# Kernel optimization log

Measured on AMD Instinct MI355X. Metric: run time of the kernel, lower is better.

The kernel has to match this reference:

```python
import math
import jax, jax.numpy as jnp
import numpy as np

RM = 100.0      # r_max
RN = 1000       # r_dsc
LMAX = 2
MATCH_FRAC = 0.1
PARA1 = 1.0
RD = RM / RN    # radial step
NE = 4096       # batch of trial energies


def setup_inputs() -> dict:
    key = jax.random.key(0)
    # small negative energies (bound-state regime) to keep the exponential
    # Numerov growth over 900 steps within fp32 range
    init_energy = -(jax.random.uniform(key, (NE,), dtype=jnp.float32) * 0.01 + 0.005)
    return {"init_energy": init_energy}


def _disc_solve(sol0, factor, limit):
    # sol0: (5, n_e, L) initial 5-point window; factor: (rn, n_e, L)
    # Numerov-style 4-step recurrence, vectorized coefficients + lax.scan
    c = 3.0 / 40.0 * RD ** 2
    idx = jnp.arange(1, limit - 5)
    f0 = factor[idx]
    f1 = factor[idx + 1]
    f2 = factor[idx + 2]
    f3 = factor[idx + 3]
    f4 = factor[idx + 4]
    denom = 1.0 - c * f4
    a = -1.0 + c * f0 / denom
    b = 2.0 + (13.0 / 15.0) * RD ** 2 * f1 / denom
    cc = -2.0 + (7.0 / 60.0) * RD ** 2 * f2 / denom
    d = 2.0 + (13.0 / 15.0) * RD ** 2 * f3 / denom

    def step(prev, coef):
        ca, cb, ccc, cd = coef
        new4 = ca * prev[1] + cb * prev[2] + ccc * prev[3] + cd * prev[4]
        new = jnp.concatenate([prev[1:], new4[None]], axis=0)  # shift window
        return new, new

    _, rest = jax.lax.scan(step, sol0, (a, b, cc, d))
    return jnp.concatenate([sol0[None], rest], axis=0)  # (limit-5, 5, n_e, L)


def _derivative(func, at):
    return (25.0 * func[at - 1] - 48.0 * func[at - 2] + 36.0 * func[at - 3]
            - 16.0 * func[at - 4] + 3.0 * func[at - 5]) / (12.0 * RD)


def _integrate(func):
    # faithful to original: integrand squares `func` again (func is u**2 here)
    M = func.shape[0] // 4 - 1
    g0 = func[0:4 * M:4]
    g1 = func[1:4 * M:4]
    g2 = func[2:4 * M:4]
    g3 = func[3:4 * M:4]
    g4 = func[4::4][:M]
    integrand = (7.0 * (g0 ** 2 + g4 ** 2) + 32.0 * (g1 ** 2 + g3 ** 2)
                 + 12.0 * g2) * (2.0 * RD / 45.0)
    return integrand.sum(axis=0)


def _forward(init_energy):
    L = LMAX + 1
    dt = init_energy.dtype
    n_e = init_energy.shape[0]
    r = jnp.linspace(RM / RN, RM, RN, dtype=dt).reshape(RN, 1, 1)
    l = jnp.arange(L, dtype=dt).reshape(1, 1, L)

    energy = jnp.broadcast_to(init_energy[:, None], (n_e, L))  # (n_e, L)
    e_val = energy[None]                                       # (1, n_e, L)
    # coulomb potential -1/r; factor: (rn, n_e, L)
    factor = l * (l + 1) / r ** 2 + PARA1 * (-e_val - 1.0 / r)

    # left (r->0) initial window: u ~ r^(l+1) + r^(l+2)/(2(l+1)) * (-para_1)
    r0 = jnp.linspace(RD, 5 * RD, 5, dtype=dt).reshape(5, 1, 1)
    u_zero_init = jnp.broadcast_to(
        r0 ** (l + 1) - r0 ** (l + 2) / (2.0 * (l + 1)) * PARA1, (5, n_e, L))

    # right (r->r_max) initial window: r * truncated spherical-bessel series
    r_inf = jnp.linspace(RM - 4 * RD, RM, 5, dtype=dt).reshape(5, 1, 1)
    fact = jnp.array([math.prod([2 * li + 1 for li in range(lm + 1)])
                      for lm in range(L)], dtype=dt)  # [1, 3, 15]
    x = r_inf * jnp.sqrt(jnp.abs(e_val))              # (5, n_e, L)
    base = x ** l / fact
    t1 = x ** 2 / 2.0 / (2 * l + 3)
    t2 = (x ** 2 / 2.0) ** 2 / (2.0 * (2 * l + 3) * (2 * l + 5))
    u_infty_init = jnp.broadcast_to(r_inf * (base * (1.0 + t1 + t2)), (5, n_e, L))

    match = int(RN * MATCH_FRAC)  # 100
    uz = _disc_solve(u_zero_init, factor, match)                     # (95, 5, n_e, L)
    ui = _disc_solve(u_infty_init, factor[::-1], RN - match)[::-1]   # (895, 5, n_e, L)
    u_zero = jnp.concatenate([uz[0], uz[:, 4]], axis=0)    # (100, n_e, L)
    u_infty = jnp.concatenate([ui[0], ui[:, 4]], axis=0)   # (900, n_e, L)

    lfunc_in = _derivative(u_zero, match) / u_zero[-1]
    # faithful: the trailing flip acts on the energy axis of the (n_e, L) result
    lfunc_out = _derivative(u_infty[::-1], RN - match)[::-1] / u_infty[0]
    integ_in = _integrate(u_zero ** 2)
    integ_out = _integrate(u_infty ** 2)
    delta = -(lfunc_out - lfunc_in) / (integ_in / u_zero[-1] ** 2
                                       + integ_out / u_infty[0] ** 2)
    return (energy + delta, u_zero, u_infty)


def reference(init_energy):
    return _forward(init_energy)
```

## Files before the change

kernel.cpp:

```cpp
#include <hip/hip_runtime.h>


namespace {
constexpr int kNE    = 4096;
constexpr int kNCH   = kNE * 3;
constexpr int kMatch = 100;
constexpr float kC   = 3.0f / 40.0f * 0.01f;
constexpr float kK1  = 13.0f / 15.0f * 0.01f;
constexpr float kK2  = 7.0f / 60.0f * 0.01f;
constexpr int kSeg        = 32;
constexpr int kCPB        = 16;
constexpr int kZeroBlocks = kNCH / 512;
constexpr int kInfBlocks  = kNCH / kCPB;
}

__device__ __forceinline__ float rcp_f(float x) { return __builtin_amdgcn_rcpf(x); }
__device__ __forceinline__ void nt_store(float v, float* p) { __builtin_nontemporal_store(v, p); }

__global__ __launch_bounds__(512) void solve_kernel(const float* __restrict__ energy,
                                                    float* __restrict__ out,
                                                    float* __restrict__ ws)
{
    __shared__ float sP[kSeg][kCPB][16];
    __shared__ float sSt[kSeg][kCPB][4];
    float* sR4 = &sP[0][0][0];
    float* sR2 = sR4 + kSeg * kCPB;

    const int bid = (int)blockIdx.x;
    const int tid = (int)threadIdx.x;
    float* uzero = out + kNCH;
    float* uinf  = out + kNCH + (size_t)kMatch * kNCH;

    if (bid < kZeroBlocks) {
        const int t  = bid * 512 + tid;
        const int l  = t % 3;
        const int ei = t / 3;
        const float e = energy[ei], negE = -e;
        const float ll1 = (float)(l * (l + 1));
        const float rdiv = (l == 0) ? 0.5f : ((l == 1) ? 0.25f : (1.0f/6.0f));
        float p0,p1,p2,p3,p4;
        {
            float pw[5];
            #pragma unroll
            for (int k = 0; k < 5; ++k) {
                float r = 0.1f * (float)(k + 1);
                float rl1 = (l == 0) ? r : ((l == 1) ? r*r : r*r*r);
                pw[k] = rl1 - (rl1 * r) * rdiv;
                nt_store(pw[k], uzero + (size_t)k * kNCH + t);
            }
            nt_store(pw[4], uzero + (size_t)5 * kNCH + t);
            p0=pw[0]; p1=pw[1]; p2=pw[2]; p3=pw[3]; p4=pw[4];
        }
        float acc4, acc2;
        {
            float q0=p0*p0, q1=p1*p1, q2=p2*p2, q3=p3*p3, q4=p4*p4;
            acc4 = 7.0f*q0*q0 + 32.0f*q1*q1 + 32.0f*q3*q3 + 14.0f*q4*q4 + 32.0f*q4*q4;
            acc2 = q2;
        }
        float f0, f1, f2, f3;
        {
            float i1 = rcp_f(0.2f), i2 = rcp_f(0.3f), i3 = rcp_f(0.4f), i4 = rcp_f(0.5f);
            f0 = fmaf(i1, fmaf(ll1, i1, -1.0f), negE);
            f1 = fmaf(i2, fmaf(ll1, i2, -1.0f), negE);
            f2 = fmaf(i3, fmaf(ll1, i3, -1.0f), negE);
            f3 = fmaf(i4, fmaf(ll1, i4, -1.0f), negE);
        }
        float* ptr = uzero + (size_t)6 * kNCH + t;
        #pragma unroll 4
        for (int j = 5; j <= 98; ++j) {
            float ri = rcp_f(fmaf((float)j, 0.1f, 0.1f));
            float f4 = fmaf(ri, fmaf(ll1, ri, -1.0f), negE);
            float iv = rcp_f(fmaf(-kC, f4, 1.0f));
            float a  = fmaf(kC  * f0, iv, -1.0f);
            float b  = fmaf(kK1 * f1, iv,  2.0f);
            float cc = fmaf(kK2 * f2, iv, -2.0f);
            float d  = fmaf(kK1 * f3, iv,  2.0f);
            float nw = fmaf(d, p4, fmaf(cc, p3, fmaf(b, p2, a * p1)));
            nt_store(nw, ptr); ptr += kNCH;
            float v2 = nw*nw, v4 = v2*v2;
            if (j <= 94) {
                int m = (j + 1) & 3;
                if (m == 2)      acc2 += v2;
                else if (m == 0) acc4 += 14.0f * v4;
                else             acc4 += 32.0f * v4;
            } else if (j == 95) {
                acc4 += 7.0f * v4;
            }
            f0 = f1; f1 = f2; f2 = f3; f3 = f4;
            p0 = p1; p1 = p2; p2 = p3; p3 = p4; p4 = nw;
        }
        float integ = fmaf(12.0f, acc2, acc4) * (2.0f * 0.1f / 45.0f);
        float deriv = fmaf(25.0f, p4, fmaf(-48.0f, p3, fmaf(36.0f, p2,
                      fmaf(-16.0f, p1, 3.0f * p0)))) * (1.0f / 1.2f);
        ws[2 * kNCH + t] = deriv / p4;
        ws[3 * kNCH + t] = integ / (p4 * p4);
        return;
    }

    const int b = bid - kZeroBlocks;
    const int g = tid & 15;
    const int s = tid >> 4;
    const int t = b * kCPB + g;
    const int l  = t % 3;
    const int ei = t / 3;
    const float e = energy[ei], negE = -e;
    const float ll1 = (float)(l * (l + 1));
    const int jstart = 5 + 28 * s;
    int j = jstart;

    float F0, F1, F2, F3;
    {
        float i0 = rcp_f(fmaf((float)(jstart - 4), -0.1f, 100.0f));
        float i1 = rcp_f(fmaf((float)(jstart - 3), -0.1f, 100.0f));
        float i2 = rcp_f(fmaf((float)(jstart - 2), -0.1f, 100.0f));
        float i3 = rcp_f(fmaf((float)(jstart - 1), -0.1f, 100.0f));
        F0 = fmaf(i0, fmaf(ll1, i0, -1.0f), negE);
        F1 = fmaf(i1, fmaf(ll1, i1, -1.0f), negE);
        F2 = fmaf(i2, fmaf(ll1, i2, -1.0f), negE);
        F3 = fmaf(i3, fmaf(ll1, i3, -1.0f), negE);
    }
    const float ff0 = F0, ff1 = F1, ff2 = F2, ff3 = F3;

    float ca, cb, cc_, cd;
#define COEF(FA,FB,FC,FD) \
    { float ri = rcp_f(fmaf((float)j, -0.1f, 100.0f)); \
      float f4 = fmaf(ri, fmaf(ll1, ri, -1.0f), negE); \
      float iv = rcp_f(fmaf(-kC, f4, 1.0f)); \
      ca  = fmaf(kC  * FA, iv, -1.0f); \
      cb  = fmaf(kK1 * FB, iv,  2.0f); \
      cc_ = fmaf(kK2 * FC, iv, -2.0f); \
      cd  = fmaf(kK1 * FD, iv,  2.0f); \
      FA = f4; }

#define MSTEP(FA,FB,FC,FD,RA,RB,RC,RD) \
    { COEF(FA,FB,FC,FD) \
      RA[0] = fmaf(cd,RD[0], fmaf(cc_,RC[0], fmaf(cb,RB[0], ca*RA[0]))); \
      RA[1] = fmaf(cd,RD[1], fmaf(cc_,RC[1], fmaf(cb,RB[1], ca*RA[1]))); \
      RA[2] = fmaf(cd,RD[2], fmaf(cc_,RC[2], fmaf(cb,RB[2], ca*RA[2]))); \
      RA[3] = fmaf(cd,RD[3], fmaf(cc_,RC[3], fmaf(cb,RB[3], ca*RA[3]))); \
      ++j; }

    if (s < kSeg - 1) {
        float ra[4] = {1,0,0,0}, rb[4] = {0,1,0,0}, rc[4] = {0,0,1,0}, rd[4] = {0,0,0,1};
        for (int it = 0; it < 7; ++it) {
            MSTEP(F0,F1,F2,F3, ra,rb,rc,rd)
            MSTEP(F1,F2,F3,F0, rb,rc,rd,ra)
            MSTEP(F2,F3,F0,F1, rc,rd,ra,rb)
            MSTEP(F3,F0,F1,F2, rd,ra,rb,rc)
        }
        float* dst = &sP[s][g][0];
        #pragma unroll
        for (int c = 0; c < 4; ++c) {
            dst[c] = ra[c]; dst[4+c] = rb[c]; dst[8+c] = rc[c]; dst[12+c] = rd[c];
        }
    }
    __syncthreads();

    if (s == 0) {
        const float se  = sqrtf(fabsf(e));
        const float rfc = (l == 0) ? 1.0f : ((l == 1) ? (1.0f/3.0f) : (1.0f/15.0f));
        const float rt1 = (l == 0) ? (1.0f/3.0f) : ((l == 1) ? (1.0f/5.0f) : (1.0f/7.0f));
        const float rt2 = (l == 0) ? (1.0f/30.0f) : ((l == 1) ? (1.0f/70.0f) : (1.0f/126.0f));
        float pw[5];
        #pragma unroll
        for (int k = 0; k < 5; ++k) {
            float rinf = 99.6f + 0.1f * (float)k;
            float x  = rinf * se;
            float xl = (l == 0) ? 1.0f : ((l == 1) ? x : x * x);
            float h  = x * x * 0.5f;
            pw[k] = rinf * (xl * rfc * (1.0f + h * rt1 + (h * h) * rt2));
        }
        nt_store(pw[4], uinf + (size_t)899 * kNCH + t);
        float st0 = pw[1], st1 = pw[2], st2 = pw[3], st3 = pw[4];
        for (int ss = 0; ss < kSeg; ++ss) {
            sSt[ss][g][0] = st0; sSt[ss][g][1] = st1;
            sSt[ss][g][2] = st2; sSt[ss][g][3] = st3;
            if (ss < kSeg - 1) {
                const float* P = &sP[ss][g][0];
                float n0 = fmaf(P[ 3],st3, fmaf(P[ 2],st2, fmaf(P[ 1],st1, P[ 0]*st0)));
                float n1 = fmaf(P[ 7],st3, fmaf(P[ 6],st2, fmaf(P[ 5],st1, P[ 4]*st0)));
                float n2 = fmaf(P[11],st3, fmaf(P[10],st2, fmaf(P[ 9],st1, P[ 8]*st0)));
                float n3 = fmaf(P[15],st3, fmaf(P[14],st2, fmaf(P[13],st1, P[12]*st0)));
                st0 = n0; st1 = n1; st2 = n2; st3 = n3;
            }
        }
    }
    __syncthreads();

    j = jstart;
    F0 = ff0; F1 = ff1; F2 = ff2; F3 = ff3;
    float p0 = sSt[s][g][0], p1 = sSt[s][g][1], p2 = sSt[s][g][2], p3 = sSt[s][g][3];
    float acc4 = 0.0f, acc2 = 0.0f;
    float* ptr = uinf + (size_t)(903 - jstart) * kNCH + t;
#define RSTEP(FA,FB,FC,FD,PA,PB,PC,PD) \
    { COEF(FA,FB,FC,FD) \
      float nw = fmaf(cd,PD, fmaf(cc_,PC, fmaf(cb,PB, ca*PA))); \
      PA = nw; nt_store(nw, ptr); ptr -= kNCH; \
      float v2 = nw*nw, v4 = v2*v2; \
      if (j >= 8) { int m = j & 3; \
        if (m == 1) acc2 += v2; \
        else acc4 += ((m == 3) ? 14.0f : 32.0f) * v4; } \
      else if (j == 7) acc4 += 7.0f * v4; \
      ++j; }

    float h0 = 0.0f;
    if (s < kSeg - 1) {
        for (int it = 0; it < 7; ++it) {
            RSTEP(F0,F1,F2,F3, p0,p1,p2,p3)
            RSTEP(F1,F2,F3,F0, p1,p2,p3,p0)
            RSTEP(F2,F3,F0,F1, p2,p3,p0,p1)
            RSTEP(F3,F0,F1,F2, p3,p0,p1,p2)
        }
    } else {
        for (int it = 0; it < 6; ++it) {
            RSTEP(F0,F1,F2,F3, p0,p1,p2,p3)
            RSTEP(F1,F2,F3,F0, p1,p2,p3,p0)
            RSTEP(F2,F3,F0,F1, p2,p3,p0,p1)
            RSTEP(F3,F0,F1,F2, p3,p0,p1,p2)
        }
        RSTEP(F0,F1,F2,F3, p0,p1,p2,p3)
        h0 = p1;
        RSTEP(F1,F2,F3,F0, p1,p2,p3,p0)
    }
    sR4[s * kCPB + g] = acc4;
    sR2[s * kCPB + g] = acc2;
    __syncthreads();

    if (s == kSeg - 1) {
        float a4 = 0.0f, a2 = 0.0f;
        #pragma unroll
        for (int ss = 0; ss < kSeg; ++ss) {
            a4 += sR4[ss * kCPB + g]; a2 += sR2[ss * kCPB + g];
        }
        float h1 = p2, h2 = p3, h3 = p0, h4 = p1;
        nt_store(h0, uinf + (size_t)0 * kNCH + t);
        nt_store(h1, uinf + (size_t)1 * kNCH + t);
        nt_store(h2, uinf + (size_t)2 * kNCH + t);
        nt_store(h3, uinf + (size_t)3 * kNCH + t);
        nt_store(h4, uinf + (size_t)4 * kNCH + t);
        float q0 = h0*h0, q1 = h1*h1, q2 = h2*h2, q3 = h3*h3, q4 = h4*h4;
        a4 += 7.0f*q0*q0 + 32.0f*q1*q1 + 32.0f*q3*q3 + 14.0f*q4*q4;
        a2 += q2;
        float integ = fmaf(12.0f, a2, a4) * (2.0f * 0.1f / 45.0f);
        float deriv = fmaf(25.0f, h0, fmaf(-48.0f, h1, fmaf(36.0f, h2,
                      fmaf(-16.0f, h3, 3.0f * h4)))) * (1.0f / 1.2f);
        ws[t]        = deriv / h0;
        ws[kNCH + t] = integ / (h0 * h0);
    }
#undef RSTEP
#undef MSTEP
#undef COEF
}

__global__ __launch_bounds__(256) void final_kernel(const float* __restrict__ energy,
                                                    const float* __restrict__ ws,
                                                    float* __restrict__ out)
{
    int t = (int)blockIdx.x * 256 + (int)threadIdx.x;
    if (t >= kNCH) return;
    int l = t % 3, ei = t / 3;
    float lf_out = ws[(kNE - 1 - ei) * 3 + l];
    float lf_in  = ws[2 * kNCH + t];
    float den    = ws[kNCH + t] + ws[3 * kNCH + t];
    out[t] = energy[ei] - (lf_out - lf_in) / den;
}

extern "C" void kernel_launch(void* const* d_in, const int* in_sizes, int n_in,
                              void* d_out, int out_size, void* d_ws, size_t ws_size,
                              hipStream_t stream) {
    (void)in_sizes; (void)n_in; (void)out_size; (void)ws_size;
    const float* energy = (const float*)d_in[0];
    float* out = (float*)d_out;
    float* ws  = (float*)d_ws;
    solve_kernel<<<kZeroBlocks + kInfBlocks, 512, 0, stream>>>(energy, out, ws);
    final_kernel<<<kNCH / 256, 256, 0, stream>>>(energy, ws, out);
}
```

Measured before the change: 92.40 us.

## Precompute radial terms in LDS, replace reciprocal with series, transpose sP, drop nontemporal stores

Builds a shared-memory table of the r-dependent potential terms per block, so the inner loops read them instead of computing two hardware reciprocals per step. The 1/(1-c*f) denominator becomes a second-order series, which relies on c*f being tiny at large r. The segment propagator matrices are stored transposed to avoid LDS bank conflicts in the serial combine, and nontemporal stores become ordinary stores. This adds a block-wide table build and sync, and slightly changes numerics.

```diff
diff --git a/kernel.cpp b/kernel.cpp
--- a/kernel.cpp
+++ b/kernel.cpp
@@ -15,15 +15,19 @@
 }
 
 __device__ __forceinline__ float rcp_f(float x) { return __builtin_amdgcn_rcpf(x); }
-__device__ __forceinline__ void nt_store(float v, float* p) { __builtin_nontemporal_store(v, p); }
+__device__ __forceinline__ float rcp_nr(float x) {
+    float r = __builtin_amdgcn_rcpf(x);
+    return fmaf(fmaf(-x, r, 1.0f), r, r);
+}
 
 __global__ __launch_bounds__(512) void solve_kernel(const float* __restrict__ energy,
                                                     float* __restrict__ out,
                                                     float* __restrict__ ws)
 {
-    __shared__ float sP[kSeg][kCPB][16];
+    __shared__ float gt[899 * 3];
+    __shared__ float sPT[16][kSeg - 1][kCPB];
     __shared__ float sSt[kSeg][kCPB][4];
-    float* sR4 = &sP[0][0][0];
+    float* sR4 = &sPT[0][0][0];
     float* sR2 = sR4 + kSeg * kCPB;
 
     const int bid = (int)blockIdx.x;
@@ -46,9 +50,9 @@
                 float r = 0.1f * (float)(k + 1);
                 float rl1 = (l == 0) ? r : ((l == 1) ? r*r : r*r*r);
                 pw[k] = rl1 - (rl1 * r) * rdiv;
-                nt_store(pw[k], uzero + (size_t)k * kNCH + t);
+                uzero[(size_t)k * kNCH + t] = pw[k];
             }
-            nt_store(pw[4], uzero + (size_t)5 * kNCH + t);
+            uzero[(size_t)5 * kNCH + t] = pw[4];
             p0=pw[0]; p1=pw[1]; p2=pw[2]; p3=pw[3]; p4=pw[4];
         }
         float acc4, acc2;
@@ -76,7 +80,7 @@
             float cc = fmaf(kK2 * f2, iv, -2.0f);
             float d  = fmaf(kK1 * f3, iv,  2.0f);
             float nw = fmaf(d, p4, fmaf(cc, p3, fmaf(b, p2, a * p1)));
-            nt_store(nw, ptr); ptr += kNCH;
+            *ptr = nw; ptr += kNCH;
             float v2 = nw*nw, v4 = v2*v2;
             if (j <= 94) {
                 int m = (j + 1) & 3;
@@ -97,6 +101,14 @@
         return;
     }
 
+    for (int j = tid; j < 899; j += 512) {
+        float ri = rcp_nr(fmaf((float)j, -0.1f, 100.0f));
+        gt[j * 3 + 0] = -ri;
+        gt[j * 3 + 1] = ri * fmaf(2.0f, ri, -1.0f);
+        gt[j * 3 + 2] = ri * fmaf(6.0f, ri, -1.0f);
+    }
+    __syncthreads();
+
     const int b = bid - kZeroBlocks;
     const int g = tid & 15;
     const int s = tid >> 4;
@@ -104,28 +116,21 @@
     const int l  = t % 3;
     const int ei = t / 3;
     const float e = energy[ei], negE = -e;
-    const float ll1 = (float)(l * (l + 1));
     const int jstart = 5 + 28 * s;
-    int j = jstart;
-
-    float F0, F1, F2, F3;
-    {
-        float i0 = rcp_f(fmaf((float)(jstart - 4), -0.1f, 100.0f));
-        float i1 = rcp_f(fmaf((float)(jstart - 3), -0.1f, 100.0f));
-        float i2 = rcp_f(fmaf((float)(jstart - 2), -0.1f, 100.0f));
-        float i3 = rcp_f(fmaf((float)(jstart - 1), -0.1f, 100.0f));
-        F0 = fmaf(i0, fmaf(ll1, i0, -1.0f), negE);
-        F1 = fmaf(i1, fmaf(ll1, i1, -1.0f), negE);
-        F2 = fmaf(i2, fmaf(ll1, i2, -1.0f), negE);
-        F3 = fmaf(i3, fmaf(ll1, i3, -1.0f), negE);
-    }
-    const float ff0 = F0, ff1 = F1, ff2 = F2, ff3 = F3;
+
+    const float ff0 = gt[(jstart - 4) * 3 + l] + negE;
+    const float ff1 = gt[(jstart - 3) * 3 + l] + negE;
+    const float ff2 = gt[(jstart - 2) * 3 + l] + negE;
+    const float ff3 = gt[(jstart - 1) * 3 + l] + negE;
+    float F0 = ff0, F1 = ff1, F2 = ff2, F3 = ff3;
+    const float* gp0 = &gt[jstart * 3 + l];
+    const float* gp = gp0;
 
     float ca, cb, cc_, cd;
 #define COEF(FA,FB,FC,FD) \
-    { float ri = rcp_f(fmaf((float)j, -0.1f, 100.0f)); \
-      float f4 = fmaf(ri, fmaf(ll1, ri, -1.0f), negE); \
-      float iv = rcp_f(fmaf(-kC, f4, 1.0f)); \
+    { float f4 = *gp + negE; gp += 3; \
+      float x  = kC * f4; \
+      float iv = fmaf(x, x, x) + 1.0f; \
       ca  = fmaf(kC  * FA, iv, -1.0f); \
       cb  = fmaf(kK1 * FB, iv,  2.0f); \
       cc_ = fmaf(kK2 * FC, iv, -2.0f); \
@@ -137,8 +142,7 @@
       RA[0] = fmaf(cd,RD[0], fmaf(cc_,RC[0], fmaf(cb,RB[0], ca*RA[0]))); \
       RA[1] = fmaf(cd,RD[1], fmaf(cc_,RC[1], fmaf(cb,RB[1], ca*RA[1]))); \
       RA[2] = fmaf(cd,RD[2], fmaf(cc_,RC[2], fmaf(cb,RB[2], ca*RA[2]))); \
-      RA[3] = fmaf(cd,RD[3], fmaf(cc_,RC[3], fmaf(cb,RB[3], ca*RA[3]))); \
-      ++j; }
+      RA[3] = fmaf(cd,RD[3], fmaf(cc_,RC[3], fmaf(cb,RB[3], ca*RA[3]))); }
 
     if (s < kSeg - 1) {
         float ra[4] = {1,0,0,0}, rb[4] = {0,1,0,0}, rc[4] = {0,0,1,0}, rd[4] = {0,0,0,1};
@@ -148,10 +152,12 @@
             MSTEP(F2,F3,F0,F1, rc,rd,ra,rb)
             MSTEP(F3,F0,F1,F2, rd,ra,rb,rc)
         }
-        float* dst = &sP[s][g][0];
         #pragma unroll
         for (int c = 0; c < 4; ++c) {
-            dst[c] = ra[c]; dst[4+c] = rb[c]; dst[8+c] = rc[c]; dst[12+c] = rd[c];
+            sPT[0*4+c][s][g] = ra[c];
+            sPT[1*4+c][s][g] = rb[c];
+            sPT[2*4+c][s][g] = rc[c];
+            sPT[3*4+c][s][g] = rd[c];
         }
     }
     __syncthreads();
@@ -170,32 +176,36 @@
             float h  = x * x * 0.5f;
             pw[k] = rinf * (xl * rfc * (1.0f + h * rt1 + (h * h) * rt2));
         }
-        nt_store(pw[4], uinf + (size_t)899 * kNCH + t);
+        uinf[(size_t)899 * kNCH + t] = pw[4];
         float st0 = pw[1], st1 = pw[2], st2 = pw[3], st3 = pw[4];
         for (int ss = 0; ss < kSeg; ++ss) {
             sSt[ss][g][0] = st0; sSt[ss][g][1] = st1;
             sSt[ss][g][2] = st2; sSt[ss][g][3] = st3;
             if (ss < kSeg - 1) {
-                const float* P = &sP[ss][g][0];
-                float n0 = fmaf(P[ 3],st3, fmaf(P[ 2],st2, fmaf(P[ 1],st1, P[ 0]*st0)));
-                float n1 = fmaf(P[ 7],st3, fmaf(P[ 6],st2, fmaf(P[ 5],st1, P[ 4]*st0)));
-                float n2 = fmaf(P[11],st3, fmaf(P[10],st2, fmaf(P[ 9],st1, P[ 8]*st0)));
-                float n3 = fmaf(P[15],st3, fmaf(P[14],st2, fmaf(P[13],st1, P[12]*st0)));
+                float n0 = fmaf(sPT[ 3][ss][g],st3, fmaf(sPT[ 2][ss][g],st2,
+                           fmaf(sPT[ 1][ss][g],st1, sPT[ 0][ss][g]*st0)));
+                float n1 = fmaf(sPT[ 7][ss][g],st3, fmaf(sPT[ 6][ss][g],st2,
+                           fmaf(sPT[ 5][ss][g],st1, sPT[ 4][ss][g]*st0)));
+                float n2 = fmaf(sPT[11][ss][g],st3, fmaf(sPT[10][ss][g],st2,
+                           fmaf(sPT[ 9][ss][g],st1, sPT[ 8][ss][g]*st0)));
+                float n3 = fmaf(sPT[15][ss][g],st3, fmaf(sPT[14][ss][g],st2,
+                           fmaf(sPT[13][ss][g],st1, sPT[12][ss][g]*st0)));
                 st0 = n0; st1 = n1; st2 = n2; st3 = n3;
             }
         }
     }
     __syncthreads();
 
-    j = jstart;
+    gp = gp0;
     F0 = ff0; F1 = ff1; F2 = ff2; F3 = ff3;
+    int j = jstart;
     float p0 = sSt[s][g][0], p1 = sSt[s][g][1], p2 = sSt[s][g][2], p3 = sSt[s][g][3];
     float acc4 = 0.0f, acc2 = 0.0f;
     float* ptr = uinf + (size_t)(903 - jstart) * kNCH + t;
 #define RSTEP(FA,FB,FC,FD,PA,PB,PC,PD) \
     { COEF(FA,FB,FC,FD) \
       float nw = fmaf(cd,PD, fmaf(cc_,PC, fmaf(cb,PB, ca*PA))); \
-      PA = nw; nt_store(nw, ptr); ptr -= kNCH; \
+      PA = nw; *ptr = nw; ptr -= kNCH; \
       float v2 = nw*nw, v4 = v2*v2; \
       if (j >= 8) { int m = j & 3; \
         if (m == 1) acc2 += v2; \
@@ -233,11 +243,11 @@
             a4 += sR4[ss * kCPB + g]; a2 += sR2[ss * kCPB + g];
         }
         float h1 = p2, h2 = p3, h3 = p0, h4 = p1;
-        nt_store(h0, uinf + (size_t)0 * kNCH + t);
-        nt_store(h1, uinf + (size_t)1 * kNCH + t);
-        nt_store(h2, uinf + (size_t)2 * kNCH + t);
-        nt_store(h3, uinf + (size_t)3 * kNCH + t);
-        nt_store(h4, uinf + (size_t)4 * kNCH + t);
+        uinf[(size_t)0 * kNCH + t] = h0;
+        uinf[(size_t)1 * kNCH + t] = h1;
+        uinf[(size_t)2 * kNCH + t] = h2;
+        uinf[(size_t)3 * kNCH + t] = h3;
+        uinf[(size_t)4 * kNCH + t] = h4;
         float q0 = h0*h0, q1 = h1*h1, q2 = h2*h2, q3 = h3*h3, q4 = h4*h4;
         a4 += 7.0f*q0*q0 + 32.0f*q1*q1 + 32.0f*q3*q3 + 14.0f*q4*q4;
         a2 += q2;
```

Result: no change. 93.13 us (+0.8%).
